# Kernel optimization log

Hardware: AMD Instinct MI355X
Metric: run time of the kernel (lower is better)

The kernel has to match this reference:

```python
import jax, jax.numpy as jnp
import numpy as np

WS = 7      # window size
SS = 3      # shift size = WS // 2
NH = 12     # num heads
EPS = 1e-5  # LayerNorm eps


def _ln(x, g, b):
    m = jnp.mean(x, axis=-1, keepdims=True)
    v = jnp.var(x, axis=-1, keepdims=True)
    return (x - m) * jax.lax.rsqrt(v + EPS) * g + b


def _rel_index(ws):
    # relative position index (N, N), N = ws*ws (static, numpy)
    coords = np.stack(np.meshgrid(np.arange(ws), np.arange(ws), indexing='ij')).reshape(2, -1)
    rel = (coords[:, :, None] - coords[:, None, :]).transpose(1, 2, 0).copy()
    rel[:, :, 0] += ws - 1
    rel[:, :, 1] += ws - 1
    rel[:, :, 0] *= 2 * ws - 1
    return rel.sum(-1)


def _attn_mask(H, W, ws, ss):
    # SW-MSA mask (nW, N, N): -100 where tokens come from different shifted regions
    img = np.zeros((H, W), np.float32)
    cnt = 0
    sls = (slice(0, -ws), slice(-ws, -ss), slice(-ss, None))
    for hs in sls:
        for wsl in sls:
            img[hs, wsl] = cnt
            cnt += 1
    win = img.reshape(H // ws, ws, W // ws, ws).transpose(0, 2, 1, 3).reshape(-1, ws * ws)
    d = win[:, None, :] - win[:, :, None]
    return np.where(d != 0, -100.0, 0.0).astype(np.float32)


def _forward(x, rel_bias_table, qkv_w, qkv_b, proj_w, proj_b,
             norm1_w, norm1_b, norm2_w, norm2_b,
             mlp_w1, mlp_b1, mlp_w2, mlp_b2, h, w):
    B, L, C = x.shape
    ws, ss, nH = WS, SS, NH
    hd = C // nH
    N = ws * ws
    scale = hd ** -0.5
    nWh, nWw = h // ws, w // ws
    nW = nWh * nWw

    shortcut = x
    y = _ln(x, norm1_w, norm1_b).reshape(B, h, w, C)
    # cyclic shift (SW-MSA)
    y = jnp.roll(y, (-ss, -ss), axis=(1, 2))
    # window partition -> (B*nW, N, C)
    y = y.reshape(B, nWh, ws, nWw, ws, C).transpose(0, 1, 3, 2, 4, 5).reshape(-1, N, C)

    qkv = (y @ qkv_w + qkv_b).reshape(-1, N, 3, nH, hd).transpose(2, 0, 3, 1, 4)
    q, k, v = qkv[0] * scale, qkv[1], qkv[2]  # (Bw, nH, N, hd)

    attn = jnp.einsum('bhnd,bhmd->bhnm', q, k)  # (Bw, nH, N, N)
    # learned relative position bias
    idx = jnp.asarray(_rel_index(ws))  # (N, N)
    bias = rel_bias_table[idx].transpose(2, 0, 1)[None]  # (1, nH, N, N)
    attn = attn + bias
    # shifted-window mask
    mask = jnp.asarray(_attn_mask(h, w, ws, ss))  # (nW, N, N)
    attn = attn.reshape(B, nW, nH, N, N) + mask[None, :, None]
    attn = jax.nn.softmax(attn.reshape(-1, nH, N, N), axis=-1)

    out = jnp.einsum('bhnm,bhmd->bhnd', attn, v).transpose(0, 2, 1, 3).reshape(-1, N, C)
    out = out @ proj_w + proj_b
    # window reverse + un-shift
    out = out.reshape(B, nWh, nWw, ws, ws, C).transpose(0, 1, 3, 2, 4, 5).reshape(B, h, w, C)
    out = jnp.roll(out, (ss, ss), axis=(1, 2)).reshape(B, L, C)

    x = shortcut + out
    y2 = _ln(x, norm2_w, norm2_b)
    mlp = jax.nn.gelu(y2 @ mlp_w1 + mlp_b1, approximate=False) @ mlp_w2 + mlp_b2
    return x + mlp


def setup_inputs() -> dict:
    key = jax.random.key(0)
    ks = jax.random.split(key, 8)
    B, H, W, C = 32, 56, 56, 384
    hid = int(C * 4.0)
    ws, nH = WS, NH
    inp = {
        'x': jax.random.normal(ks[0], (B, H * W, C), jnp.float32),
        'rel_bias_table': 0.02 * jax.random.normal(ks[1], ((2 * ws - 1) * (2 * ws - 1), nH), jnp.float32),
        'qkv_w': 0.02 * jax.random.normal(ks[2], (C, 3 * C), jnp.float32),
        'qkv_b': jnp.zeros((3 * C,), jnp.float32),
        'proj_w': 0.02 * jax.random.normal(ks[3], (C, C), jnp.float32),
        'proj_b': jnp.zeros((C,), jnp.float32),
        'norm1_w': jnp.ones((C,), jnp.float32),
        'norm1_b': jnp.zeros((C,), jnp.float32),
        'norm2_w': jnp.ones((C,), jnp.float32),
        'norm2_b': jnp.zeros((C,), jnp.float32),
        'mlp_w1': 0.02 * jax.random.normal(ks[4], (C, hid), jnp.float32),
        'mlp_b1': jnp.zeros((hid,), jnp.float32),
        'mlp_w2': 0.02 * jax.random.normal(ks[5], (hid, C), jnp.float32),
        'mlp_b2': jnp.zeros((C,), jnp.float32),
        'h': H,
        'w': W,
    }
    return inp


def reference(x, rel_bias_table, qkv_w, qkv_b, proj_w, proj_b,
              norm1_w, norm1_b, norm2_w, norm2_b,
              mlp_w1, mlp_b1, mlp_w2, mlp_b2, h, w):
    return _forward(x, rel_bias_table, qkv_w, qkv_b, proj_w, proj_b,
                    norm1_w, norm1_b, norm2_w, norm2_b,
                    mlp_w1, mlp_b1, mlp_w2, mlp_b2, h, w)
```

## Files before the change

### kernel.cpp

```cpp
#include <hip/hip_runtime.h>

typedef unsigned short u16;
typedef unsigned int u32;
typedef short s8v __attribute__((ext_vector_type(8)));
typedef float f4 __attribute__((ext_vector_type(4)));

#define GL16(g, l) __builtin_amdgcn_global_load_lds((const __attribute__((address_space(1))) u32*)(g), (__attribute__((address_space(3))) u32*)(l), 16, 0, 0)

__device__ __forceinline__ u16 f2bf(float f){
  u32 u = __builtin_bit_cast(u32, f);
  u32 r = u + 0x7fffu + ((u >> 16) & 1u);
  return (u16)(r >> 16);
}
__device__ __forceinline__ float bf2f(u16 u){
  u32 x = ((u32)u) << 16;
  return __builtin_bit_cast(float, x);
}

__device__ __forceinline__ u32 pk_bf16(float lo, float hi){
  u32 r;
  asm("v_cvt_pk_bf16_f32 %0, %1, %2" : "=v"(r) : "v"(lo), "v"(hi));
  return r;
}

__device__ __forceinline__ float gelu_f(float x){
  float y = fabsf(x) * 0.70710678118654752f;
  float t = __builtin_amdgcn_rcpf(1.f + 0.3275911f*y);
  float p = ((((1.061405429f*t - 1.453152027f)*t + 1.421413741f)*t - 0.284496736f)*t + 0.254829592f)*t;
  float er = 1.f - p*__expf(-y*y);
  er = copysignf(er, x);
  return 0.5f*x*(1.f + er);
}

__device__ __forceinline__ int win_to_src(int orow){
  int wi = orow / 49;
  int n  = orow - wi*49;
  int b  = wi >> 6;
  int wq = wi & 63;
  int wh = wq >> 3, ww = wq & 7;
  int r = n / 7, c = n - r*7;
  int hh = wh*7 + r + 3; if (hh >= 56) hh -= 56;
  int wp = ww*7 + c + 3; if (wp >= 56) wp -= 56;
  return (b*56 + hh)*56 + wp;
}

__global__ void sentinel_kernel(float* o){ o[0] = 1.0e9f; }

__global__ void transpose_cast(const float* __restrict__ in, u16* __restrict__ out,
                               int K, int N, float scale, int scale_lim){
  __shared__ float tile[16][17];
  int kb = blockIdx.x*16, nb = blockIdx.y*16;
  int tx = threadIdx.x, ty = threadIdx.y;
  int k = kb + ty, n = nb + tx;
  tile[ty][tx] = (k < K && n < N) ? in[(size_t)k*N + n] : 0.f;
  __syncthreads();
  int on = nb + ty, ok = kb + tx;
  if (on < N && ok < K){
    float v = tile[tx][ty];
    if (on < scale_lim) v *= scale;
    out[(size_t)on*K + ok] = f2bf(v);
  }
}

__global__ void scale_bias(const float* __restrict__ in, float* __restrict__ out,
                           int n, float s, int lim){
  int i = blockIdx.x*256 + threadIdx.x;
  if (i < n) out[i] = in[i] * (i < lim ? s : 1.f);
}

__global__ void build_biasmask(const float* __restrict__ table, u16* __restrict__ bm){
  int wq = blockIdx.x, h = blockIdx.y;
  int wh = wq >> 3, ww = wq & 7;
  u16* o = bm + (size_t)(wq*12 + h) * 4096;
  for (int i = threadIdx.x; i < 4096; i += 256){
    int m = i >> 6, n = i & 63;
    float v;
    if (m < 49 && n < 49){
      int rm = m/7, cm = m - rm*7;
      int rn = n/7, cn = n - rn*7;
      int idx = (rm - rn + 6)*13 + (cm - cn + 6);
      v = table[idx*12 + h];
      int ym = wh*7 + rm, xm = ww*7 + cm;
      int yn = wh*7 + rn, xn = ww*7 + cn;
      int lm = (ym < 49 ? 0 : (ym < 53 ? 1 : 2))*3 + (xm < 49 ? 0 : (xm < 53 ? 1 : 2));
      int ln = (yn < 49 ? 0 : (yn < 53 ? 1 : 2))*3 + (xn < 49 ? 0 : (xn < 53 ? 1 : 2));
      if (lm != ln) v += -100.f;
    } else {
      v = -1e9f;
    }
    o[i] = f2bf(v);
  }
}

template<bool GATHER>
__global__ __launch_bounds__(256) void ln_kernel(const float* __restrict__ x,
    const float* __restrict__ g, const float* __restrict__ b,
    u16* __restrict__ y, int nrows)
{
  int row = blockIdx.x*4 + (threadIdx.x >> 6);
  int lane = threadIdx.x & 63;
  if (row >= nrows) return;
  int src = GATHER ? win_to_src(row) : row;
  const float* xr = x + (size_t)src*384;
  float v[6];
  float s = 0.f, s2 = 0.f;
  #pragma unroll
  for (int p = 0; p < 3; p++){
    float2 t = *(const float2*)(xr + p*128 + lane*2);
    v[p*2] = t.x; v[p*2+1] = t.y;
    s += t.x + t.y; s2 += t.x*t.x + t.y*t.y;
  }
  #pragma unroll
  for (int off = 32; off; off >>= 1){
    s  += __shfl_xor(s,  off);
    s2 += __shfl_xor(s2, off);
  }
  float mean = s * (1.f/384.f);
  float var  = s2 * (1.f/384.f) - mean*mean;
  float rs   = rsqrtf(var + 1e-5f);
  u16* yr = y + (size_t)row*384;
  #pragma unroll
  for (int p = 0; p < 3; p++){
    int c = p*128 + lane*2;
    float a0 = (v[p*2]   - mean)*rs*g[c]   + b[c];
    float a1 = (v[p*2+1] - mean)*rs*g[c+1] + b[c+1];
    *(u32*)(yr + c) = pk_bf16(a0, a1);
  }
}

template<int MODE, int NF>
__global__ __launch_bounds__(256) void gemm_bf16(
    const u16* __restrict__ A, const u16* __restrict__ Bt,
    const float* __restrict__ bias, const float* __restrict__ resid,
    void* __restrict__ outp, int K, int N, int gn)
{
  constexpr int TN = NF * 32;
  __shared__ u16 As[2][128*32];
  __shared__ u16 Bs[2][TN*32];
  const int tid  = threadIdx.x;
  const int lane = tid & 63, wv = tid >> 6;
  const int wr = wv >> 1, wc = wv & 1;
  const int l15 = lane & 15, lhi = lane >> 4;
  const int sw2 = l15 & 3;

  int total = gridDim.x;
  int flat  = blockIdx.x;
  int swz   = flat;
  if ((total & 7) == 0){
    int cpx = total >> 3;
    swz = (flat & 7)*cpx + (flat >> 3);
  }
  int bm = swz / gn, bn = swz - bm*gn;
  const size_t m0 = (size_t)bm * 128;
  const int n0 = bn * TN;

  f4 acc[4][NF] = {};

  auto stage = [&](int buf, int kt){
    #pragma unroll
    for (int it = 0; it < 2; it++){
      int c = it*256 + tid;
      int row = c >> 2;
      int col = ((c & 3) ^ (row & 3)) * 8;
      const u16* ga = A + (m0 + (size_t)row)*K + kt*32 + col;
      GL16(ga, &As[buf][(it*256 + wv*64)*8]);
    }
    #pragma unroll
    for (int it = 0; it < 2; it++){
      int c = it*256 + tid;
      int row = c >> 2;
      int col = ((c & 3) ^ (row & 3)) * 8;
      const u16* gb = Bt + ((size_t)n0 + row)*K + kt*32 + col;
      GL16(gb, &Bs[buf][(it*256 + wv*64)*8]);
    }
  };

  const int nk = K >> 5;
  stage(0, 0);
  for (int kt = 0; kt < nk; kt++){
    const int cur = kt & 1;
    if (kt + 1 < nk){
      stage(cur ^ 1, kt + 1);
      asm volatile("s_waitcnt vmcnt(4)" ::: "memory");
    } else {
      asm volatile("s_waitcnt vmcnt(0)" ::: "memory");
    }
    __builtin_amdgcn_s_barrier();
    s8v a[4], bb[NF];
    #pragma unroll
    for (int mi = 0; mi < 4; mi++)
      a[mi] = *(const s8v*)&As[cur][(wr*64 + mi*16 + l15)*32 + (lhi ^ sw2)*8];
    #pragma unroll
    for (int ni = 0; ni < NF; ni++)
      bb[ni] = *(const s8v*)&Bs[cur][(wc*NF*16 + ni*16 + l15)*32 + (lhi ^ sw2)*8];
    #pragma unroll
    for (int mi = 0; mi < 4; mi++)
      #pragma unroll
      for (int ni = 0; ni < NF; ni++)
        acc[mi][ni] = __builtin_amdgcn_mfma_f32_16x16x32_bf16(bb[ni], a[mi], acc[mi][ni], 0, 0, 0);
    asm volatile("s_waitcnt lgkmcnt(0)" ::: "memory");
    __builtin_amdgcn_s_barrier();
  }

  #pragma unroll
  for (int mi = 0; mi < 4; mi++){
    int m = (int)m0 + wr*64 + mi*16 + l15;
    int src = 0;
    if constexpr (MODE == 1) src = win_to_src(m);
    #pragma unroll
    for (int ni = 0; ni < NF; ni++){
      int n = n0 + wc*NF*16 + ni*16 + lhi*4;
      f4 v = acc[mi][ni];
      float4 b4 = *(const float4*)(bias + n);
      v[0] += b4.x; v[1] += b4.y; v[2] += b4.z; v[3] += b4.w;
      if constexpr (MODE == 0){
        uint2 pk; pk.x = pk_bf16(v[0], v[1]); pk.y = pk_bf16(v[2], v[3]);
        *(uint2*)((u16*)outp + (size_t)m*N + n) = pk;
      } else if constexpr (MODE == 1){
        const float4 r4 = *(const float4*)(resid + (size_t)src*384 + n);
        float4 o4; o4.x = v[0]+r4.x; o4.y = v[1]+r4.y; o4.z = v[2]+r4.z; o4.w = v[3]+r4.w;
        *(float4*)((float*)outp + (size_t)src*384 + n) = o4;
      } else if constexpr (MODE == 2){
        uint2 pk;
        pk.x = pk_bf16(gelu_f(v[0]), gelu_f(v[1]));
        pk.y = pk_bf16(gelu_f(v[2]), gelu_f(v[3]));
        *(uint2*)((u16*)outp + (size_t)m*N + n) = pk;
      } else {
        float4* o = (float4*)((float*)outp + (size_t)m*N + n);
        float4 c4 = *o;
        c4.x += v[0]; c4.y += v[1]; c4.z += v[2]; c4.w += v[3];
        *o = c4;
      }
    }
  }
}

__global__ __launch_bounds__(256) void attn_kernel(
    const u16* __restrict__ qkv, const u16* __restrict__ bm, u16* __restrict__ ao)
{
  const int wi = blockIdx.x;
  const int hg = blockIdx.y;
  const int wv = threadIdx.x >> 6, lane = threadIdx.x & 63;
  const int h = hg*4 + wv;
  const int l15 = lane & 15, lhi = lane >> 4;
  const int wq = wi & 63;

  __shared__ u16 Plds[4][64*72];
  __shared__ u16 Vlds[4][32*72];

  const size_t base = (size_t)wi * 49 * 1152;
  s8v z8 = (s8v)0;

  #pragma unroll
  for (int i = 0; i < 4; i++){
    int n  = i*16 + (lane >> 2);
    int d8 = (lane & 3)*8;
    s8v v = (n < 49) ? *(const s8v*)&qkv[base + (size_t)n*1152 + 768 + h*32 + d8] : z8;
    #pragma unroll
    for (int j = 0; j < 8; j++)
      Vlds[wv][(d8 + j)*72 + n] = (u16)v[j];
  }

  s8v aQ[4], bK[4];
  #pragma unroll
  for (int mi = 0; mi < 4; mi++){
    int rowq = mi*16 + l15;
    aQ[mi] = (rowq < 49) ? *(const s8v*)&qkv[base + (size_t)rowq*1152 +   0 + h*32 + lhi*8] : z8;
    bK[mi] = (rowq < 49) ? *(const s8v*)&qkv[base + (size_t)rowq*1152 + 384 + h*32 + lhi*8] : z8;
  }
  f4 zf = {0.f, 0.f, 0.f, 0.f};
  f4 s[4][4];
  #pragma unroll
  for (int mi = 0; mi < 4; mi++)
    #pragma unroll
    for (int ni = 0; ni < 4; ni++)
      s[mi][ni] = __builtin_amdgcn_mfma_f32_16x16x32_bf16(aQ[mi], bK[ni], zf, 0, 0, 0);

  const u16* bmp = bm + (size_t)(wq*12 + h) * 4096;
  #pragma unroll
  for (int mi = 0; mi < 4; mi++)
    #pragma unroll
    for (int ni = 0; ni < 4; ni++)
      #pragma unroll
      for (int r = 0; r < 4; r++){
        int m = mi*16 + lhi*4 + r, n = ni*16 + l15;
        s[mi][ni][r] += bf2f(bmp[m*64 + n]);
      }

  #pragma unroll
  for (int mi = 0; mi < 4; mi++){
    #pragma unroll
    for (int r = 0; r < 4; r++){
      float mx = fmaxf(fmaxf(s[mi][0][r], s[mi][1][r]), fmaxf(s[mi][2][r], s[mi][3][r]));
      mx = fmaxf(mx, __shfl_xor(mx, 1));
      mx = fmaxf(mx, __shfl_xor(mx, 2));
      mx = fmaxf(mx, __shfl_xor(mx, 4));
      mx = fmaxf(mx, __shfl_xor(mx, 8));
      float sum = 0.f;
      #pragma unroll
      for (int ni = 0; ni < 4; ni++){
        float p = __expf(s[mi][ni][r] - mx);
        s[mi][ni][r] = p; sum += p;
      }
      sum += __shfl_xor(sum, 1);
      sum += __shfl_xor(sum, 2);
      sum += __shfl_xor(sum, 4);
      sum += __shfl_xor(sum, 8);
      float inv = 1.f / sum;
      #pragma unroll
      for (int ni = 0; ni < 4; ni++) s[mi][ni][r] *= inv;
    }
  }

  #pragma unroll
  for (int mi = 0; mi < 4; mi++)
    #pragma unroll
    for (int ni = 0; ni < 4; ni++)
      #pragma unroll
      for (int r = 0; r < 4; r++){
        int m = mi*16 + lhi*4 + r, n = ni*16 + l15;
        Plds[wv][m*72 + n] = f2bf(s[mi][ni][r]);
      }
  __syncthreads();

  f4 o[4][2] = {};
  #pragma unroll
  for (int ks = 0; ks < 2; ks++){
    s8v aP[4], bV[2];
    #pragma unroll
    for (int mi = 0; mi < 4; mi++)
      aP[mi] = *(const s8v*)&Plds[wv][(mi*16 + l15)*72 + ks*32 + lhi*8];
    #pragma unroll
    for (int di = 0; di < 2; di++)
      bV[di] = *(const s8v*)&Vlds[wv][(di*16 + l15)*72 + ks*32 + lhi*8];
    #pragma unroll
    for (int mi = 0; mi < 4; mi++)
      #pragma unroll
      for (int di = 0; di < 2; di++)
        o[mi][di] = __builtin_amdgcn_mfma_f32_16x16x32_bf16(aP[mi], bV[di], o[mi][di], 0, 0, 0);
  }

  #pragma unroll
  for (int mi = 0; mi < 4; mi++)
    #pragma unroll
    for (int di = 0; di < 2; di++)
      #pragma unroll
      for (int r = 0; r < 4; r++){
        int m = mi*16 + lhi*4 + r;
        if (m < 49){
          int d = di*16 + l15;
          ao[((size_t)wi*49 + m)*384 + h*32 + d] = f2bf(o[mi][di][r]);
        }
      }
}

extern "C" void kernel_launch(void* const* d_in, const int* in_sizes, int n_in,
                              void* d_out, int out_size, void* d_ws, size_t ws_size,
                              hipStream_t stream)
{
  const float* x      = (const float*)d_in[0];
  const float* table  = (const float*)d_in[1];
  const float* qkv_w  = (const float*)d_in[2];
  const float* qkv_b  = (const float*)d_in[3];
  const float* proj_w = (const float*)d_in[4];
  const float* proj_b = (const float*)d_in[5];
  const float* n1w    = (const float*)d_in[6];
  const float* n1b    = (const float*)d_in[7];
  const float* n2w    = (const float*)d_in[8];
  const float* n2b    = (const float*)d_in[9];
  const float* w1     = (const float*)d_in[10];
  const float* b1     = (const float*)d_in[11];
  const float* w2     = (const float*)d_in[12];
  const float* b2     = (const float*)d_in[13];
  float* out = (float*)d_out;

  const size_t M = 100352;
  const float SC = 0.17677669529663689f;

  const size_t R1 = M * 1536 * 2;
  const size_t R2 = M * 384 * 2;
  const size_t R3 = (size_t)64*12*64*64*2;
  const size_t WT = (size_t)(1152*384 + 384*384 + 1536*384 + 384*1536) * 2;
  const size_t BB = 1152 * 4;
  const size_t needed = R1 + R2 + R3 + WT + BB;
  if (ws_size < needed){
    sentinel_kernel<<<1, 1, 0, stream>>>(out);
    return;
  }

  char* p = (char*)d_ws;
  u16*   qkvbuf = (u16*)p;
  u16*   ybuf   = (u16*)(p + R1);
  u16*   bmbuf  = (u16*)(p + R1 + R2);
  u16*   qkvT   = (u16*)(p + R1 + R2 + R3);
  u16*   projT  = qkvT  + (size_t)1152*384;
  u16*   w1T    = projT + (size_t)384*384;
  u16*   w2T    = w1T   + (size_t)1536*384;
  float* qkvb_s = (float*)(p + R1 + R2 + R3 + WT);

  transpose_cast<<<dim3(24, 72),  dim3(16,16), 0, stream>>>(qkv_w,  qkvT, 384, 1152, SC, 384);
  transpose_cast<<<dim3(24, 24),  dim3(16,16), 0, stream>>>(proj_w, projT, 384, 384, 1.f, 0);
  transpose_cast<<<dim3(24, 96),  dim3(16,16), 0, stream>>>(w1,     w1T,  384, 1536, 1.f, 0);
  transpose_cast<<<dim3(96, 24),  dim3(16,16), 0, stream>>>(w2,     w2T,  1536, 384, 1.f, 0);
  scale_bias<<<5, 256, 0, stream>>>(qkv_b, qkvb_s, 1152, SC, 384);
  build_biasmask<<<dim3(64, 12), 256, 0, stream>>>(table, bmbuf);

  ln_kernel<true><<<M/4, 256, 0, stream>>>(x, n1w, n1b, ybuf, (int)M);

  gemm_bf16<0,4><<<784*9, 256, 0, stream>>>(ybuf, qkvT, qkvb_s, nullptr, qkvbuf, 384, 1152, 9);

  attn_kernel<<<dim3(2048, 3), 256, 0, stream>>>(qkvbuf, bmbuf, ybuf);

  gemm_bf16<1,4><<<784*3, 256, 0, stream>>>(ybuf, projT, proj_b, x, out, 384, 384, 3);

  ln_kernel<false><<<M/4, 256, 0, stream>>>(out, n2w, n2b, ybuf, (int)M);

  gemm_bf16<2,4><<<784*12, 256, 0, stream>>>(ybuf, w1T, b1, nullptr, qkvbuf, 384, 1536, 12);

  gemm_bf16<3,4><<<784*3, 256, 0, stream>>>(qkvbuf, w2T, b2, nullptr, out, 1536, 384, 3);
}
```

Baseline: 1.054 ms.

## Double GEMM K-tile depth and stage bf16 epilogue through LDS for coalesced stores

The GEMM K tile grows from 32 to 64. The LDS XOR swizzle widens to 8 chunks, and each barrier-synchronized iteration now issues two MFMA sub-steps. This halves the number of barriers and waits per K loop, at the cost of twice the LDS buffer size, which may lower occupancy. For the bf16-output modes (plain and GELU), the accumulators are written into a padded LDS tile and then stored to global memory as full 16-byte row-contiguous chunks, replacing scattered 8-byte stores. The padded tile (128x136) is larger than the As buffer, so it relies on the shared memory that follows As.

```diff
diff --git a/kernel.cpp b/kernel.cpp
--- a/kernel.cpp
+++ b/kernel.cpp
@@ -135,13 +135,13 @@
     void* __restrict__ outp, int K, int N, int gn)
 {
   constexpr int TN = NF * 32;
-  __shared__ u16 As[2][128*32];
-  __shared__ u16 Bs[2][TN*32];
+  __shared__ u16 As[2][128*64];
+  __shared__ u16 Bs[2][TN*64];
   const int tid  = threadIdx.x;
   const int lane = tid & 63, wv = tid >> 6;
   const int wr = wv >> 1, wc = wv & 1;
   const int l15 = lane & 15, lhi = lane >> 4;
-  const int sw2 = l15 & 3;
+  const int sw  = l15 & 7;
 
   int total = gridDim.x;
   int flat  = blockIdx.x;
@@ -158,78 +158,107 @@
 
   auto stage = [&](int buf, int kt){
     #pragma unroll
-    for (int it = 0; it < 2; it++){
+    for (int it = 0; it < 4; it++){
       int c = it*256 + tid;
-      int row = c >> 2;
-      int col = ((c & 3) ^ (row & 3)) * 8;
-      const u16* ga = A + (m0 + (size_t)row)*K + kt*32 + col;
+      int row = c >> 3;
+      int col = (((c & 7) ^ (row & 7))) * 8;
+      const u16* ga = A + (m0 + (size_t)row)*K + kt*64 + col;
       GL16(ga, &As[buf][(it*256 + wv*64)*8]);
     }
     #pragma unroll
-    for (int it = 0; it < 2; it++){
+    for (int it = 0; it < NF; it++){
       int c = it*256 + tid;
-      int row = c >> 2;
-      int col = ((c & 3) ^ (row & 3)) * 8;
-      const u16* gb = Bt + ((size_t)n0 + row)*K + kt*32 + col;
+      int row = c >> 3;
+      int col = (((c & 7) ^ (row & 7))) * 8;
+      const u16* gb = Bt + ((size_t)n0 + row)*K + kt*64 + col;
       GL16(gb, &Bs[buf][(it*256 + wv*64)*8]);
     }
   };
 
-  const int nk = K >> 5;
+  const int nk = K >> 6;
   stage(0, 0);
   for (int kt = 0; kt < nk; kt++){
     const int cur = kt & 1;
     if (kt + 1 < nk){
       stage(cur ^ 1, kt + 1);
-      asm volatile("s_waitcnt vmcnt(4)" ::: "memory");
+      asm volatile("s_waitcnt vmcnt(8)" ::: "memory");
     } else {
       asm volatile("s_waitcnt vmcnt(0)" ::: "memory");
     }
     __builtin_amdgcn_s_barrier();
-    s8v a[4], bb[NF];
-    #pragma unroll
-    for (int mi = 0; mi < 4; mi++)
-      a[mi] = *(const s8v*)&As[cur][(wr*64 + mi*16 + l15)*32 + (lhi ^ sw2)*8];
-    #pragma unroll
-    for (int ni = 0; ni < NF; ni++)
-      bb[ni] = *(const s8v*)&Bs[cur][(wc*NF*16 + ni*16 + l15)*32 + (lhi ^ sw2)*8];
-    #pragma unroll
-    for (int mi = 0; mi < 4; mi++)
+    #pragma unroll
+    for (int kk = 0; kk < 2; kk++){
+      s8v a[4], bb[NF];
+      #pragma unroll
+      for (int mi = 0; mi < 4; mi++)
+        a[mi] = *(const s8v*)&As[cur][(wr*64 + mi*16 + l15)*64 + ((kk*4 + lhi) ^ sw)*8];
       #pragma unroll
       for (int ni = 0; ni < NF; ni++)
-        acc[mi][ni] = __builtin_amdgcn_mfma_f32_16x16x32_bf16(bb[ni], a[mi], acc[mi][ni], 0, 0, 0);
+        bb[ni] = *(const s8v*)&Bs[cur][(wc*NF*16 + ni*16 + l15)*64 + ((kk*4 + lhi) ^ sw)*8];
+      #pragma unroll
+      for (int mi = 0; mi < 4; mi++)
+        #pragma unroll
+        for (int ni = 0; ni < NF; ni++)
+          acc[mi][ni] = __builtin_amdgcn_mfma_f32_16x16x32_bf16(bb[ni], a[mi], acc[mi][ni], 0, 0, 0);
+    }
     asm volatile("s_waitcnt lgkmcnt(0)" ::: "memory");
     __builtin_amdgcn_s_barrier();
   }
 
-  #pragma unroll
-  for (int mi = 0; mi < 4; mi++){
-    int m = (int)m0 + wr*64 + mi*16 + l15;
-    int src = 0;
-    if constexpr (MODE == 1) src = win_to_src(m);
-    #pragma unroll
-    for (int ni = 0; ni < NF; ni++){
-      int n = n0 + wc*NF*16 + ni*16 + lhi*4;
-      f4 v = acc[mi][ni];
-      float4 b4 = *(const float4*)(bias + n);
-      v[0] += b4.x; v[1] += b4.y; v[2] += b4.z; v[3] += b4.w;
-      if constexpr (MODE == 0){
-        uint2 pk; pk.x = pk_bf16(v[0], v[1]); pk.y = pk_bf16(v[2], v[3]);
-        *(uint2*)((u16*)outp + (size_t)m*N + n) = pk;
-      } else if constexpr (MODE == 1){
-        const float4 r4 = *(const float4*)(resid + (size_t)src*384 + n);
-        float4 o4; o4.x = v[0]+r4.x; o4.y = v[1]+r4.y; o4.z = v[2]+r4.z; o4.w = v[3]+r4.w;
-        *(float4*)((float*)outp + (size_t)src*384 + n) = o4;
-      } else if constexpr (MODE == 2){
-        uint2 pk;
-        pk.x = pk_bf16(gelu_f(v[0]), gelu_f(v[1]));
-        pk.y = pk_bf16(gelu_f(v[2]), gelu_f(v[3]));
-        *(uint2*)((u16*)outp + (size_t)m*N + n) = pk;
-      } else {
-        float4* o = (float4*)((float*)outp + (size_t)m*N + n);
-        float4 c4 = *o;
-        c4.x += v[0]; c4.y += v[1]; c4.z += v[2]; c4.w += v[3];
-        *o = c4;
+  if constexpr (MODE == 0 || MODE == 2){
+    u16* tile = (u16*)&As[0][0];
+    #pragma unroll
+    for (int mi = 0; mi < 4; mi++){
+      int ml = wr*64 + mi*16 + l15;
+      #pragma unroll
+      for (int ni = 0; ni < NF; ni++){
+        int nl = wc*NF*16 + ni*16 + lhi*4;
+        f4 v = acc[mi][ni];
+        float4 b4 = *(const float4*)(bias + n0 + nl);
+        v[0] += b4.x; v[1] += b4.y; v[2] += b4.z; v[3] += b4.w;
+        u32 p0, p1;
+        if constexpr (MODE == 2){
+          p0 = pk_bf16(gelu_f(v[0]), gelu_f(v[1]));
+          p1 = pk_bf16(gelu_f(v[2]), gelu_f(v[3]));
+        } else {
+          p0 = pk_bf16(v[0], v[1]);
+          p1 = pk_bf16(v[2], v[3]);
+        }
+        *(u32*)&tile[ml*136 + nl]     = p0;
+        *(u32*)&tile[ml*136 + nl + 2] = p1;
+      }
+    }
+    __syncthreads();
+    int rr = tid >> 4;
+    int cc = (tid & 15) * 8;
+    #pragma unroll
+    for (int pass = 0; pass < 8; pass++){
+      int row = rr + pass*16;
+      uint4 val = *(const uint4*)&tile[row*136 + cc];
+      *(uint4*)((u16*)outp + ((size_t)((int)m0 + row))*N + n0 + cc) = val;
+    }
+  } else {
+    #pragma unroll
+    for (int mi = 0; mi < 4; mi++){
+      int m = (int)m0 + wr*64 + mi*16 + l15;
+      int src = 0;
+      if constexpr (MODE == 1) src = win_to_src(m);
+      #pragma unroll
+      for (int ni = 0; ni < NF; ni++){
+        int n = n0 + wc*NF*16 + ni*16 + lhi*4;
+        f4 v = acc[mi][ni];
+        float4 b4 = *(const float4*)(bias + n);
+        v[0] += b4.x; v[1] += b4.y; v[2] += b4.z; v[3] += b4.w;
+        if constexpr (MODE == 1){
+          const float4 r4 = *(const float4*)(resid + (size_t)src*384 + n);
+          float4 o4; o4.x = v[0]+r4.x; o4.y = v[1]+r4.y; o4.z = v[2]+r4.z; o4.w = v[3]+r4.w;
+          *(float4*)((float*)outp + (size_t)src*384 + n) = o4;
+        } else {
+          float4* o = (float4*)((float*)outp + (size_t)m*N + n);
+          float4 c4 = *o;
+          c4.x += v[0]; c4.y += v[1]; c4.z += v[2]; c4.w += v[3];
+          *o = c4;
+        }
       }
     }
   }
```

Result: faster. 969.5 us (-8.0%).
